# Optimization experiments

Hardware: AMD Instinct MI355X
Metric: run time of the kernel (lower is better)

## Reference

```python
import jax, jax.numpy as jnp
import numpy as np

NUM_NODES = 1_000_000
EMB_DIM = 128
BATCH = 1024
WALK_LEN = 40
WINDOW = 5
NEG_SIZE = 5
NEG_WEIGHT = 1.0


def _make_pair_idx(L, W):
    src, dst = [], []
    for i in range(L):
        for j in range(max(0, i - W), i):
            src.append(j); dst.append(i)
        for j in range(i + 1, min(L, i + 1 + W)):
            src.append(j); dst.append(i)
    return np.asarray(src, np.int32), np.asarray(dst, np.int32)

_IDX_SRC, _IDX_DST = _make_pair_idx(WALK_LEN, WINDOW)  # [370] each
N_PAIRS_PER_WALK = _IDX_SRC.shape[0]


def setup_inputs() -> dict:
    key = jax.random.key(0)
    k1, k2, k3, k4 = jax.random.split(key, 4)
    init_range = 1.0 / EMB_DIM
    node_embed = jax.random.normal(k1, (NUM_NODES, EMB_DIM), jnp.float32) * init_range
    context_embed = jax.random.normal(k2, (NUM_NODES, EMB_DIM), jnp.float32) * init_range
    batch_walk = jax.random.randint(k3, (BATCH, WALK_LEN), 0, NUM_NODES, jnp.int32)
    n_neg = BATCH * N_PAIRS_PER_WALK * NEG_SIZE
    neg_dst_idx = jax.random.randint(k4, (n_neg,), 0, BATCH * WALK_LEN, jnp.int32)
    return {
        "node_embed": node_embed,
        "context_embed": context_embed,
        "batch_walk": batch_walk,
        "neg_dst_idx": neg_dst_idx,
    }


def reference(node_embed, context_embed, batch_walk, neg_dst_idx):
    B, L = batch_walk.shape
    flat = batch_walk.reshape(-1)                       # [B*L]
    node_e = node_embed[flat]                           # [B*L, D] gather
    ctx_e = context_embed[flat]                         # [B*L, D] gather

    offs = (jnp.arange(B, dtype=jnp.int32) * L)[:, None]
    src = (offs + jnp.asarray(_IDX_SRC)[None, :]).reshape(-1)  # [B*P]
    dst = (offs + jnp.asarray(_IDX_DST)[None, :]).reshape(-1)  # [B*P]

    pos_score = jnp.sum(node_e[src] * ctx_e[dst], axis=1)
    pos_score = jnp.clip(pos_score, -6.0, 6.0)
    pos_loss = jnp.mean(-jax.nn.log_sigmoid(pos_score))

    neg_src = jnp.repeat(dst, NEG_SIZE)                 # each pos dst repeated
    neg_score = jnp.sum(node_e[neg_src] * ctx_e[neg_dst_idx], axis=1)
    neg_score = jnp.clip(neg_score, -6.0, 6.0)
    neg_loss = jnp.mean(-jax.nn.log_sigmoid(-neg_score)) * NEG_SIZE * NEG_WEIGHT

    return pos_loss + neg_loss
```

## Files before the change

### kernel.cpp

```cpp
#include <hip/hip_runtime.h>

#define NN   1000000
#define D    128
#define DV4  32
#define BATCH 1024
#define LW   40
#define WIN  5
#define NP   370
#define NEG  5
#define NPB  (NP * NEG)
#define NPAIR_TOT (BATCH * NP)

struct Tab { short src[NP]; short dst[NP]; };
constexpr Tab mk_tab() {
  Tab t{};
  int n = 0;
  for (int i = 0; i < LW; i++) {
    int lo = i - WIN; if (lo < 0) lo = 0;
    for (int j = lo; j < i; j++) { t.src[n] = (short)j; t.dst[n] = (short)i; n++; }
    int hi = i + 1 + WIN; if (hi > LW) hi = LW;
    for (int j = i + 1; j < hi; j++) { t.src[n] = (short)j; t.dst[n] = (short)i; n++; }
  }
  return t;
}
__constant__ Tab g_tab = mk_tab();

__global__ __launch_bounds__(256) void gather_ctx(
    const float4* __restrict__ ctx, const int* __restrict__ walk,
    float4* __restrict__ out) {
  int g = blockIdx.x * blockDim.x + threadIdx.x;
  int p = g >> 5;
  int c = g & 31;
  int idx = walk[p];
  out[p * DV4 + c] = ctx[(long long)idx * DV4 + c];
}

__global__ __launch_bounds__(256) void sgns_kernel(
    const float4* __restrict__ node_embed,
    const float4* __restrict__ ctx_embed,
    const int* __restrict__ walk,
    const int* __restrict__ neg_idx,
    const float4* __restrict__ ctxg,
    float* __restrict__ out) {
  __shared__ float4 sNode[LW * DV4];
  __shared__ float4 sCtx[LW * DV4];

  const int b = blockIdx.x;
  const int tid = threadIdx.x;

  for (int e = tid; e < LW * DV4; e += 256) {
    int row = e >> 5;
    int c = e & 31;
    int idx = walk[b * LW + row];
    sNode[e] = node_embed[(long long)idx * DV4 + c];
    if (ctxg) sCtx[e] = ctxg[(size_t)(b * LW + row) * DV4 + c];
    else      sCtx[e] = ctx_embed[(long long)idx * DV4 + c];
  }
  __syncthreads();

  const int grp = tid >> 5;
  const int l = tid & 31;
  float acc = 0.f;

  for (int k = grp; k < NP; k += 8) {
    int s = g_tab.src[k];
    int d = g_tab.dst[k];
    float4 a = sNode[s * DV4 + l];
    float4 c = sCtx[d * DV4 + l];
    float p = a.x * c.x + a.y * c.y + a.z * c.z + a.w * c.w;
    p += __shfl_xor(p, 1);  p += __shfl_xor(p, 2);  p += __shfl_xor(p, 4);
    p += __shfl_xor(p, 8);  p += __shfl_xor(p, 16);
    if (l == 0) {
      float sc = fminf(fmaxf(p, -6.f), 6.f);
      acc += __logf(1.f + __expf(-sc));
    }
  }

  const int nb = b * NPB;
  for (int t = grp; t < NPB; t += 8) {
    int j = neg_idx[nb + t];
    int d = g_tab.dst[t / NEG];
    float4 a = sNode[d * DV4 + l];
    float4 c;
    if (ctxg) c = ctxg[(size_t)j * DV4 + l];
    else      c = ctx_embed[(long long)walk[j] * DV4 + l];
    float p = a.x * c.x + a.y * c.y + a.z * c.z + a.w * c.w;
    p += __shfl_xor(p, 1);  p += __shfl_xor(p, 2);  p += __shfl_xor(p, 4);
    p += __shfl_xor(p, 8);  p += __shfl_xor(p, 16);
    if (l == 0) {
      float sc = fminf(fmaxf(p, -6.f), 6.f);
      acc += __logf(1.f + __expf(sc));
    }
  }

  acc += __shfl_xor(acc, 1);  acc += __shfl_xor(acc, 2);  acc += __shfl_xor(acc, 4);
  acc += __shfl_xor(acc, 8);  acc += __shfl_xor(acc, 16); acc += __shfl_xor(acc, 32);
  __syncthreads();
  float* sRed = (float*)sNode;
  if ((tid & 63) == 0) sRed[tid >> 6] = acc;
  __syncthreads();
  if (tid == 0) {
    float s = sRed[0] + sRed[1] + sRed[2] + sRed[3];
    atomicAdd(out, s * (1.f / (float)NPAIR_TOT));
  }
}

extern "C" void kernel_launch(void* const* d_in, const int* in_sizes, int n_in,
                              void* d_out, int out_size, void* d_ws, size_t ws_size,
                              hipStream_t stream) {
  const float* node_embed = (const float*)d_in[0];
  const float* ctx_embed  = (const float*)d_in[1];
  const int*   walk       = (const int*)d_in[2];
  const int*   neg        = (const int*)d_in[3];
  float* out = (float*)d_out;

  hipMemsetAsync(d_out, 0, sizeof(float), stream);

  const size_t need = (size_t)BATCH * LW * D * sizeof(float);
  float4* ctxg = nullptr;
  if (ws_size >= need) {
    ctxg = (float4*)d_ws;
    int total = BATCH * LW * DV4;
    gather_ctx<<<total / 256, 256, 0, stream>>>(
        (const float4*)ctx_embed, walk, ctxg);
  }

  sgns_kernel<<<BATCH, 256, 0, stream>>>(
      (const float4*)node_embed, (const float4*)ctx_embed, walk, neg, ctxg, out);
}
```

Baseline: 973.9 us.

## Use 512-thread blocks, stage negative indices in LDS, batch four neg gathers per group

Blocks grow from 256 to 512 threads, so each walk gets 16 groups of 32 lanes. The context rows are no longer copied into shared memory; positive pairs read them straight from the gathered workspace. Negative indices are preloaded into shared memory, and the negative loop issues four independent global row loads per iteration to raise memory-level parallelism and hide gather latency. This costs more registers and reduction code, and it reads the positive context rows repeatedly from global memory or L2.

Result: faster. 882.0 us (-9.4%).

```diff
diff --git a/kernel.cpp b/kernel.cpp
--- a/kernel.cpp
+++ b/kernel.cpp
@@ -35,7 +35,16 @@
   out[p * DV4 + c] = ctx[(long long)idx * DV4 + c];
 }
 
-__global__ __launch_bounds__(256) void sgns_kernel(
+__device__ __forceinline__ float dot4(float4 a, float4 c) {
+  return a.x * c.x + a.y * c.y + a.z * c.z + a.w * c.w;
+}
+__device__ __forceinline__ float red32(float p) {
+  p += __shfl_xor(p, 1);  p += __shfl_xor(p, 2);  p += __shfl_xor(p, 4);
+  p += __shfl_xor(p, 8);  p += __shfl_xor(p, 16);
+  return p;
+}
+
+__global__ __launch_bounds__(512) void sgns_kernel(
     const float4* __restrict__ node_embed,
     const float4* __restrict__ ctx_embed,
     const int* __restrict__ walk,
@@ -43,50 +52,65 @@
     const float4* __restrict__ ctxg,
     float* __restrict__ out) {
   __shared__ float4 sNode[LW * DV4];
-  __shared__ float4 sCtx[LW * DV4];
+  __shared__ int sIdx[NPB];
 
   const int b = blockIdx.x;
   const int tid = threadIdx.x;
 
-  for (int e = tid; e < LW * DV4; e += 256) {
+  for (int e = tid; e < LW * DV4; e += 512) {
     int row = e >> 5;
     int c = e & 31;
     int idx = walk[b * LW + row];
     sNode[e] = node_embed[(long long)idx * DV4 + c];
-    if (ctxg) sCtx[e] = ctxg[(size_t)(b * LW + row) * DV4 + c];
-    else      sCtx[e] = ctx_embed[(long long)idx * DV4 + c];
   }
+  for (int t = tid; t < NPB; t += 512) sIdx[t] = neg_idx[b * NPB + t];
   __syncthreads();
 
   const int grp = tid >> 5;
   const int l = tid & 31;
   float acc = 0.f;
 
-  for (int k = grp; k < NP; k += 8) {
+  const float4* cwalk = ctxg ? (ctxg + (size_t)b * LW * DV4) : nullptr;
+  for (int k = grp; k < NP; k += 16) {
     int s = g_tab.src[k];
     int d = g_tab.dst[k];
     float4 a = sNode[s * DV4 + l];
-    float4 c = sCtx[d * DV4 + l];
-    float p = a.x * c.x + a.y * c.y + a.z * c.z + a.w * c.w;
-    p += __shfl_xor(p, 1);  p += __shfl_xor(p, 2);  p += __shfl_xor(p, 4);
-    p += __shfl_xor(p, 8);  p += __shfl_xor(p, 16);
+    const float4* crow = cwalk ? (cwalk + d * DV4)
+                               : (ctx_embed + (long long)walk[b * LW + d] * DV4);
+    float p = red32(dot4(a, crow[l]));
     if (l == 0) {
       float sc = fminf(fmaxf(p, -6.f), 6.f);
       acc += __logf(1.f + __expf(-sc));
     }
   }
 
-  const int nb = b * NPB;
-  for (int t = grp; t < NPB; t += 8) {
-    int j = neg_idx[nb + t];
-    int d = g_tab.dst[t / NEG];
-    float4 a = sNode[d * DV4 + l];
-    float4 c;
-    if (ctxg) c = ctxg[(size_t)j * DV4 + l];
-    else      c = ctx_embed[(long long)walk[j] * DV4 + l];
-    float p = a.x * c.x + a.y * c.y + a.z * c.z + a.w * c.w;
-    p += __shfl_xor(p, 1);  p += __shfl_xor(p, 2);  p += __shfl_xor(p, 4);
-    p += __shfl_xor(p, 8);  p += __shfl_xor(p, 16);
+  int t = grp;
+  for (; t + 48 < NPB; t += 64) {
+    int j0 = sIdx[t], j1 = sIdx[t + 16], j2 = sIdx[t + 32], j3 = sIdx[t + 48];
+    const float4* r0 = ctxg ? (ctxg + (size_t)j0 * DV4) : (ctx_embed + (long long)walk[j0] * DV4);
+    const float4* r1 = ctxg ? (ctxg + (size_t)j1 * DV4) : (ctx_embed + (long long)walk[j1] * DV4);
+    const float4* r2 = ctxg ? (ctxg + (size_t)j2 * DV4) : (ctx_embed + (long long)walk[j2] * DV4);
+    const float4* r3 = ctxg ? (ctxg + (size_t)j3 * DV4) : (ctx_embed + (long long)walk[j3] * DV4);
+    float4 c0 = r0[l], c1 = r1[l], c2 = r2[l], c3 = r3[l];
+    float4 a0 = sNode[g_tab.dst[t / NEG] * DV4 + l];
+    float4 a1 = sNode[g_tab.dst[(t + 16) / NEG] * DV4 + l];
+    float4 a2 = sNode[g_tab.dst[(t + 32) / NEG] * DV4 + l];
+    float4 a3 = sNode[g_tab.dst[(t + 48) / NEG] * DV4 + l];
+    float p0 = red32(dot4(a0, c0));
+    float p1 = red32(dot4(a1, c1));
+    float p2 = red32(dot4(a2, c2));
+    float p3 = red32(dot4(a3, c3));
+    float sel = (l == 0) ? p0 : (l == 1) ? p1 : (l == 2) ? p2 : p3;
+    if (l < 4) {
+      float sc = fminf(fmaxf(sel, -6.f), 6.f);
+      acc += __logf(1.f + __expf(sc));
+    }
+  }
+  for (; t < NPB; t += 16) {
+    int j = sIdx[t];
+    const float4* r = ctxg ? (ctxg + (size_t)j * DV4) : (ctx_embed + (long long)walk[j] * DV4);
+    float4 a = sNode[g_tab.dst[t / NEG] * DV4 + l];
+    float p = red32(dot4(a, r[l]));
     if (l == 0) {
       float sc = fminf(fmaxf(p, -6.f), 6.f);
       acc += __logf(1.f + __expf(sc));
@@ -100,7 +124,8 @@
   if ((tid & 63) == 0) sRed[tid >> 6] = acc;
   __syncthreads();
   if (tid == 0) {
-    float s = sRed[0] + sRed[1] + sRed[2] + sRed[3];
+    float s = 0.f;
+    for (int w = 0; w < 8; w++) s += sRed[w];
     atomicAdd(out, s * (1.f / (float)NPAIR_TOT));
   }
 }
@@ -125,6 +150,6 @@
         (const float4*)ctx_embed, walk, ctxg);
   }
 
-  sgns_kernel<<<BATCH, 256, 0, stream>>>(
+  sgns_kernel<<<BATCH, 512, 0, stream>>>(
       (const float4*)node_embed, (const float4*)ctx_embed, walk, neg, ctxg, out);
 }
```
